# Performance work log

Measured on AMD Instinct MI355X. Metric: run time of the kernel, lower is better.

Reference implementation:

```python
import jax, jax.numpy as jnp
import numpy as np

B, H, L, PRED_LEN = 512, 512, 2, 256


def setup_inputs() -> dict:
    key = jax.random.key(0)
    ks = jax.random.split(key, 12)
    s = 1.0 / np.sqrt(H)  # PyTorch LSTM init scale
    f32 = jnp.float32
    return {
        "h": jax.random.normal(ks[0], (L, B, H), f32),
        "c": jax.random.normal(ks[1], (L, B, H), f32),
        "W_ih0": jax.random.normal(ks[2], (4 * H, 1), f32) * s,
        "W_hh0": jax.random.normal(ks[3], (4 * H, H), f32) * s,
        "b_ih0": jax.random.normal(ks[4], (4 * H,), f32) * s,
        "b_hh0": jax.random.normal(ks[5], (4 * H,), f32) * s,
        "W_ih1": jax.random.normal(ks[6], (4 * H, H), f32) * s,
        "W_hh1": jax.random.normal(ks[7], (4 * H, H), f32) * s,
        "b_ih1": jax.random.normal(ks[8], (4 * H,), f32) * s,
        "b_hh1": jax.random.normal(ks[9], (4 * H,), f32) * s,
        "fc_w": jax.random.normal(ks[10], (1, H), f32) * s,
        "fc_b": jax.random.normal(ks[11], (1,), f32) * s,
        "pred_len": PRED_LEN,
    }


def _lstm_cell(x, h, c, W_ih, W_hh, b_ih, b_hh):
    # PyTorch gate order: i, f, g, o
    gates = x @ W_ih.T + h @ W_hh.T + (b_ih + b_hh)
    i, f, g, o = jnp.split(gates, 4, axis=-1)
    c_new = jax.nn.sigmoid(f) * c + jax.nn.sigmoid(i) * jnp.tanh(g)
    h_new = jax.nn.sigmoid(o) * jnp.tanh(c_new)
    return h_new, c_new


def reference(h, c, W_ih0, W_hh0, b_ih0, b_hh0, W_ih1, W_hh1, b_ih1, b_hh1,
              fc_w, fc_b, pred_len):
    params = ((W_ih0, W_hh0, b_ih0, b_hh0), (W_ih1, W_hh1, b_ih1, b_hh1))
    Bsz = h.shape[1]

    def step(carry, _):
        x, hs, cs = carry  # x: (B,1); hs, cs: (L,B,H)
        inp = x
        new_h, new_c = [], []
        for l in range(len(params)):
            hn, cn = _lstm_cell(inp, hs[l], cs[l], *params[l])
            new_h.append(hn)
            new_c.append(cn)
            inp = hn
        pred = inp @ fc_w.T + fc_b  # (B,1)
        return (pred, jnp.stack(new_h), jnp.stack(new_c)), pred[:, 0]

    x0 = jnp.zeros((Bsz, 1), h.dtype)  # torch.zeros(B,1,1) start token
    _, preds = jax.lax.scan(step, (x0, h, c), None, length=pred_len)
    return preds.T  # (B, pred_len)
```

## Files before the change

kernel.cpp:

```cpp
#include <hip/hip_runtime.h>
#include <hip/hip_bf16.h>


#define B_ 512
#define H_ 512
#define T_ 256
#define NWG 256
#define NTHR 512

typedef _Float16 half8_t __attribute__((ext_vector_type(8)));
typedef _Float16 half4_t __attribute__((ext_vector_type(4)));
typedef _Float16 half2_t __attribute__((ext_vector_type(2)));
typedef float floatx4 __attribute__((ext_vector_type(4)));

#define W16_BYTES  (3u * 4u * H_ * H_ * 2u)
#define HBUF_ELEMS (B_ * H_)
#define HBUF_BYTES (HBUF_ELEMS * 2u)
#define H0_OFF   ((size_t)W16_BYTES)
#define H1_OFF   (H0_OFF + 2 * HBUF_BYTES)
#define BAR_OFF  (H1_OFF + 2 * HBUF_BYTES)
#define PART_OFF (BAR_OFF + 2048)

__device__ __forceinline__ float sigm_(float x) { return 1.0f / (1.0f + __expf(-x)); }
__device__ __forceinline__ float tanh_(float x) { return 1.0f - 2.0f / (1.0f + __expf(2.0f * x)); }

__global__ void prep_weights(const float* __restrict__ whh0,
                             const float* __restrict__ wih1,
                             const float* __restrict__ whh1,
                             _Float16* __restrict__ w16) {
    const int QM = (4 * H_ * H_) / 4;
    int i = blockIdx.x * blockDim.x + threadIdx.x;
    if (i >= 3 * QM) return;
    const float* src; int base;
    if (i < QM)          { src = whh0; base = 0; }
    else if (i < 2 * QM) { src = wih1; base = QM; }
    else                 { src = whh1; base = 2 * QM; }
    float4 v = ((const float4*)src)[i - base];
    half4_t h;
    h[0] = (_Float16)v.x; h[1] = (_Float16)v.y; h[2] = (_Float16)v.z; h[3] = (_Float16)v.w;
    ((half4_t*)w16)[i] = h;
}

__global__ void prep_state(const float* __restrict__ h_in,
                           _Float16* __restrict__ H0, _Float16* __restrict__ H1) {
    int i = blockIdx.x * blockDim.x + threadIdx.x;
    float4 a = ((const float4*)h_in)[i];
    float4 b = ((const float4*)h_in)[(B_ * H_) / 4 + i];
    half4_t ha, hb;
    ha[0] = (_Float16)a.x; ha[1] = (_Float16)a.y; ha[2] = (_Float16)a.z; ha[3] = (_Float16)a.w;
    hb[0] = (_Float16)b.x; hb[1] = (_Float16)b.y; hb[2] = (_Float16)b.z; hb[3] = (_Float16)b.w;
    ((half4_t*)H0)[i] = ha;
    ((half4_t*)H1)[i] = hb;
}

#define GLL16(gptr, lptr) __builtin_amdgcn_global_load_lds( \
    (const __attribute__((address_space(1))) unsigned int*)(gptr), \
    (__attribute__((address_space(3))) unsigned int*)(lptr), 16, 0, 0x01)

__device__ __forceinline__ void stage_rows(const char* gsrc, char* lbuf, int wv, int lane) {
#pragma unroll
    for (int i = 0; i < 8; ++i) {
        int row = wv * 8 + i;
        const char* g_ = gsrc + row * 1024 + (((lane ^ (row & 7)) & 63) << 4);
        GLL16(g_, lbuf + row * 1024);
    }
}

__device__ __forceinline__ floatx4 load16_sc0(const float* p) {
    floatx4 v;
    asm volatile("global_load_dwordx4 %0, %1, off sc0" : "=v"(v) : "v"(p) : "memory");
    return v;
}

#define LBAR() asm volatile("s_waitcnt lgkmcnt(0)\n\ts_barrier" ::: "memory")
#define FBAR() asm volatile("s_waitcnt vmcnt(0) lgkmcnt(0)\n\ts_barrier" ::: "memory")

__launch_bounds__(NTHR)
__global__ void lstm_decode(
    const float* __restrict__ c_in,
    const float* __restrict__ wih0, const float* __restrict__ bih0,
    const float* __restrict__ bhh0,
    const float* __restrict__ bih1, const float* __restrict__ bhh1,
    const float* __restrict__ fcw, const float* __restrict__ fcb,
    const _Float16* __restrict__ w16,
    _Float16* __restrict__ Hs0, _Float16* __restrict__ Hs1,
    int* __restrict__ bar, float* __restrict__ part,
    float* __restrict__ outp)
{
    __shared__ __align__(16) char bufA[65536];
    __shared__ __align__(16) char bufB[65536];
    __shared__ float gbuf[4][64][20];
    __shared__ float xrow[64];
    __shared__ int sh_bt, sh_ct;

    const int tid  = (int)threadIdx.x;
    const int lane = tid & 63;
    const int wv   = tid >> 6;
    const int g    = wv & 3;
    const int kh   = wv >> 2;
    const int cl   = lane & 15;
    const int kg   = lane >> 4;

    if (tid == 0) {
        unsigned int xcc;
        asm volatile("s_getreg_b32 %0, hwreg(HW_REG_XCC_ID)" : "=s"(xcc));
        int mybt = (int)(xcc & 7u);
        int rank = atomicAdd(&bar[256 + mybt], 1);
        sh_bt = mybt;
        sh_ct = rank & 31;
    }
    __syncthreads();
    const int bt = sh_bt;
    const int ct = sh_ct;

    const int n = g * H_ + ct * 16 + cl;
    half8_t wf0[8], wf1[8], wf2[8];
    {
        const _Float16* r0 = w16 + (size_t)n * H_ + kh * 256 + kg * 8;
        const _Float16* r1 = r0 + 4 * H_ * H_;
        const _Float16* r2 = r0 + 8 * H_ * H_;
#pragma unroll
        for (int ksg = 0; ksg < 8; ++ksg) {
            wf0[ksg] = *(const half8_t*)(r0 + ksg * 32);
            wf1[ksg] = *(const half8_t*)(r1 + ksg * 32);
            wf2[ksg] = *(const half8_t*)(r2 + ksg * 32);
        }
    }
    const float b0   = bih0[n] + bhh0[n];
    const float b1   = bih1[n] + bhh1[n];
    const float wx   = wih0[n];
    const float fcb0 = fcb[0];

    const int erow = tid >> 3;
    const int ecol = (tid & 7) * 2;
    float c0a, c0b, c1a, c1b;
    {
        size_t base0 = (size_t)(bt * 64 + erow) * H_ + ct * 16 + ecol;
        c0a = c_in[base0];                     c0b = c_in[base0 + 1];
        c1a = c_in[(size_t)B_ * H_ + base0];   c1b = c_in[(size_t)B_ * H_ + base0 + 1];
    }
    const float2 fcv = *(const float2*)(fcw + ct * 16 + ecol);

    const int abase = cl * 1024 + kh * 512 + kg * 16;
    const int axor  = (cl & 7) << 4;

    int* flagg   = bar + bt * 32;
    float* partg = part + bt * 2048;
    int ep = 0;

#define PASSH(bufc, wf, acc, M0, M1) do {                                     \
    _Pragma("unroll")                                                         \
    for (int ksg = 0; ksg < 8; ++ksg) {                                       \
        _Pragma("unroll")                                                     \
        for (int mt = (M0); mt <= (M1); ++mt) {                               \
            int a_ = (abase + mt * 16384 + ksg * 64) ^ axor;                  \
            half8_t av_ = *(const half8_t*)((bufc) + a_);                     \
            acc[mt] = __builtin_amdgcn_mfma_f32_16x16x32_f16(av_, (wf)[ksg],  \
                                                             acc[mt], 0, 0, 0); \
        }                                                                     \
    }                                                                         \
} while (0)

    floatx4 accG0[4], accG1[4];
    floatx4 pv;

    if (tid < 64) xrow[tid] = 0.f;
    stage_rows((const char*)Hs0 + (size_t)bt * 64 * 1024, bufB, wv, lane);
    stage_rows((const char*)Hs1 + (size_t)bt * 64 * 1024, bufA, wv, lane);
    FBAR();
#pragma unroll
    for (int mt = 0; mt < 4; ++mt) accG0[mt] = (floatx4)0.f;
    PASSH(bufB, wf0, accG0, 0, 3);

    for (int t = 0; t < T_; ++t) {
        const size_t pnxt = (size_t)((t + 1) & 1);
        _Float16* h0w = Hs0 + pnxt * HBUF_ELEMS;
        _Float16* h1w = Hs1 + pnxt * HBUF_ELEMS;

        if (t > 0) {
            asm volatile("s_waitcnt vmcnt(8)" : "+v"(pv) :: "memory");
            float xs = (pv[0] + pv[1]) + (pv[2] + pv[3]);
            xs += __shfl_xor(xs, 1);
            xs += __shfl_xor(xs, 2);
            xs += __shfl_xor(xs, 4);
            xs += fcb0;
            if ((tid & 7) == 0) {
                xrow[tid >> 3] = xs;
                if (ct == 0) outp[(size_t)(bt * 64 + (tid >> 3)) * T_ + (t - 1)] = xs;
            }
        }
        LBAR();

        if (kh == 0) {
#pragma unroll
            for (int mt = 0; mt < 4; ++mt)
#pragma unroll
                for (int r = 0; r < 4; ++r)
                    gbuf[g][mt * 16 + kg * 4 + r][cl] =
                        accG0[mt][r] + __builtin_fmaf(xrow[mt * 16 + kg * 4 + r], wx, b0);
        }
        LBAR();
        if (kh == 1) {
#pragma unroll
            for (int mt = 0; mt < 4; ++mt)
#pragma unroll
                for (int r = 0; r < 4; ++r)
                    gbuf[g][mt * 16 + kg * 4 + r][cl] += accG0[mt][r];
        }
        LBAR();

        {
            float2 iv = *(const float2*)&gbuf[0][erow][ecol];
            float2 fv = *(const float2*)&gbuf[1][erow][ecol];
            float2 gv = *(const float2*)&gbuf[2][erow][ecol];
            float2 ov = *(const float2*)&gbuf[3][erow][ecol];
            float ca = sigm_(fv.x) * c0a + sigm_(iv.x) * tanh_(gv.x);
            float cb = sigm_(fv.y) * c0b + sigm_(iv.y) * tanh_(gv.y);
            c0a = ca; c0b = cb;
            half2_t hh;
            hh[0] = (_Float16)(sigm_(ov.x) * tanh_(ca));
            hh[1] = (_Float16)(sigm_(ov.y) * tanh_(cb));
            *(half2_t*)(h0w + (size_t)(bt * 64 + erow) * H_ + ct * 16 + ecol) = hh;
        }

        ++ep;
        FBAR();
        if (tid == 0)
            __hip_atomic_store(&flagg[ct], ep, __ATOMIC_RELAXED, __HIP_MEMORY_SCOPE_AGENT);

#pragma unroll
        for (int mt = 0; mt < 4; ++mt) {
            if (kh == 0) {
#pragma unroll
                for (int r = 0; r < 4; ++r) accG1[mt][r] = b1;
            } else {
                accG1[mt] = (floatx4)0.f;
            }
        }
        PASSH(bufA, wf2, accG1, 0, 1);

        if (wv == 0) {
            for (;;) {
                int v_ = __hip_atomic_load(&flagg[lane & 31], __ATOMIC_RELAXED,
                                           __HIP_MEMORY_SCOPE_AGENT);
                if (__all(v_ >= ep)) break;
            }
        }
        __syncthreads();

        stage_rows((const char*)h0w + (size_t)bt * 64 * 1024, bufB, wv, lane);

        PASSH(bufA, wf2, accG1, 2, 3);

        FBAR();

        PASSH(bufB, wf1, accG1, 0, 3);

        if (kh == 0) {
#pragma unroll
            for (int mt = 0; mt < 4; ++mt)
#pragma unroll
                for (int r = 0; r < 4; ++r)
                    gbuf[g][mt * 16 + kg * 4 + r][cl] = accG1[mt][r];
        }
        LBAR();
        if (kh == 1) {
#pragma unroll
            for (int mt = 0; mt < 4; ++mt)
#pragma unroll
                for (int r = 0; r < 4; ++r)
                    gbuf[g][mt * 16 + kg * 4 + r][cl] += accG1[mt][r];
        }
        LBAR();

        {
            float2 iv = *(const float2*)&gbuf[0][erow][ecol];
            float2 fv = *(const float2*)&gbuf[1][erow][ecol];
            float2 gv = *(const float2*)&gbuf[2][erow][ecol];
            float2 ov = *(const float2*)&gbuf[3][erow][ecol];
            float ca = sigm_(fv.x) * c1a + sigm_(iv.x) * tanh_(gv.x);
            float cb = sigm_(fv.y) * c1b + sigm_(iv.y) * tanh_(gv.y);
            c1a = ca; c1b = cb;
            float ha = sigm_(ov.x) * tanh_(ca);
            float hb = sigm_(ov.y) * tanh_(cb);
            half2_t hh; hh[0] = (_Float16)ha; hh[1] = (_Float16)hb;
            *(half2_t*)(h1w + (size_t)(bt * 64 + erow) * H_ + ct * 16 + ecol) = hh;
            float ps = __builtin_fmaf(ha, fcv.x, hb * fcv.y);
            ps += __shfl_xor(ps, 1);
            ps += __shfl_xor(ps, 2);
            ps += __shfl_xor(ps, 4);
            if ((tid & 7) == 0)
                partg[(tid >> 3) * 32 + ct] = ps;
        }

        ++ep;
        FBAR();
        if (tid == 0)
            __hip_atomic_store(&flagg[ct], ep, __ATOMIC_RELAXED, __HIP_MEMORY_SCOPE_AGENT);

#pragma unroll
        for (int mt = 0; mt < 4; ++mt) accG0[mt] = (floatx4)0.f;
        PASSH(bufB, wf0, accG0, 0, 1);

        if (wv == 0) {
            for (;;) {
                int v_ = __hip_atomic_load(&flagg[lane & 31], __ATOMIC_RELAXED,
                                           __HIP_MEMORY_SCOPE_AGENT);
                if (__all(v_ >= ep)) break;
            }
        }
        __syncthreads();

        pv = load16_sc0(partg + (tid >> 3) * 32 + (tid & 7) * 4);
        stage_rows((const char*)Hs1 + pnxt * HBUF_BYTES + (size_t)bt * 64 * 1024,
                   bufA, wv, lane);

        PASSH(bufB, wf0, accG0, 2, 3);
    }

    {
        asm volatile("s_waitcnt vmcnt(8)" : "+v"(pv) :: "memory");
        float xs = (pv[0] + pv[1]) + (pv[2] + pv[3]);
        xs += __shfl_xor(xs, 1);
        xs += __shfl_xor(xs, 2);
        xs += __shfl_xor(xs, 4);
        xs += fcb0;
        if ((tid & 7) == 0 && ct == 0)
            outp[(size_t)(bt * 64 + (tid >> 3)) * T_ + (T_ - 1)] = xs;
    }
#undef PASSH
#undef LBAR
#undef FBAR
}

extern "C" void kernel_launch(void* const* d_in, const int* in_sizes, int n_in,
                              void* d_out, int out_size, void* d_ws, size_t ws_size,
                              hipStream_t stream) {
    const float* h_in = (const float*)d_in[0];
    const float* c_in = (const float*)d_in[1];
    const float* wih0 = (const float*)d_in[2];
    const float* whh0 = (const float*)d_in[3];
    const float* bih0 = (const float*)d_in[4];
    const float* bhh0 = (const float*)d_in[5];
    const float* wih1 = (const float*)d_in[6];
    const float* whh1 = (const float*)d_in[7];
    const float* bih1 = (const float*)d_in[8];
    const float* bhh1 = (const float*)d_in[9];
    const float* fcw  = (const float*)d_in[10];
    const float* fcb  = (const float*)d_in[11];
    float* out = (float*)d_out;

    char* ws = (char*)d_ws;
    _Float16* w16 = (_Float16*)ws;
    _Float16* Hs0 = (_Float16*)(ws + H0_OFF);
    _Float16* Hs1 = (_Float16*)(ws + H1_OFF);
    int* bar      = (int*)(ws + BAR_OFF);
    float* part   = (float*)(ws + PART_OFF);

    (void)hipMemsetAsync(bar, 0, 2048, stream);

    {
        const int n4 = 3 * (4 * H_ * H_) / 4;
        prep_weights<<<(n4 + 255) / 256, 256, 0, stream>>>(whh0, wih1, whh1, w16);
    }
    prep_state<<<(B_ * H_ / 4) / 256, 256, 0, stream>>>(h_in, Hs0, Hs1);

    lstm_decode<<<NWG, NTHR, 0, stream>>>(c_in, wih0, bih0, bhh0, bih1, bhh1,
                                          fcw, fcb, w16, Hs0, Hs1, bar, part, out);
}
```

Baseline: 1.809 ms.

## Remap waves to two gates per quarter-K so each LDS A-fragment feeds two MFMAs

```diff
diff --git a/kernel.cpp b/kernel.cpp
--- a/kernel.cpp
+++ b/kernel.cpp
@@ -89,17 +89,19 @@
 {
     __shared__ __align__(16) char bufA[65536];
     __shared__ __align__(16) char bufB[65536];
-    __shared__ float gbuf[4][64][20];
     __shared__ float xrow[64];
     __shared__ int sh_bt, sh_ct;
 
     const int tid  = (int)threadIdx.x;
     const int lane = tid & 63;
     const int wv   = tid >> 6;
-    const int g    = wv & 3;
-    const int kh   = wv >> 2;
+    const int gp_  = wv & 1;
+    const int kq   = wv >> 1;
     const int cl   = lane & 15;
     const int kg   = lane >> 4;
+
+    float (*gbB)[2][64][20] = (float (*)[2][64][20])bufB;
+    float (*gbA)[2][64][20] = (float (*)[2][64][20])bufA;
 
     if (tid == 0) {
         unsigned int xcc;
@@ -113,22 +115,24 @@
     const int bt = sh_bt;
     const int ct = sh_ct;
 
-    const int n = g * H_ + ct * 16 + cl;
-    half8_t wf0[8], wf1[8], wf2[8];
-    {
-        const _Float16* r0 = w16 + (size_t)n * H_ + kh * 256 + kg * 8;
+    half8_t wf0[2][4], wf1[2][4], wf2[2][4];
+    float b0v[2], b1v[2], wxv[2];
+#pragma unroll
+    for (int g = 0; g < 2; ++g) {
+        const int n = (gp_ + 2 * g) * H_ + ct * 16 + cl;
+        const _Float16* r0 = w16 + (size_t)n * H_ + kq * 128 + kg * 8;
         const _Float16* r1 = r0 + 4 * H_ * H_;
         const _Float16* r2 = r0 + 8 * H_ * H_;
 #pragma unroll
-        for (int ksg = 0; ksg < 8; ++ksg) {
-            wf0[ksg] = *(const half8_t*)(r0 + ksg * 32);
-            wf1[ksg] = *(const half8_t*)(r1 + ksg * 32);
-            wf2[ksg] = *(const half8_t*)(r2 + ksg * 32);
-        }
-    }
-    const float b0   = bih0[n] + bhh0[n];
-    const float b1   = bih1[n] + bhh1[n];
-    const float wx   = wih0[n];
+        for (int ksg = 0; ksg < 4; ++ksg) {
+            wf0[g][ksg] = *(const half8_t*)(r0 + ksg * 32);
+            wf1[g][ksg] = *(const half8_t*)(r1 + ksg * 32);
+            wf2[g][ksg] = *(const half8_t*)(r2 + ksg * 32);
+        }
+        b0v[g] = bih0[n] + bhh0[n];
+        b1v[g] = bih1[n] + bhh1[n];
+        wxv[g] = wih0[n];
+    }
     const float fcb0 = fcb[0];
 
     const int erow = tid >> 3;
@@ -141,27 +145,29 @@
     }
     const float2 fcv = *(const float2*)(fcw + ct * 16 + ecol);
 
-    const int abase = cl * 1024 + kh * 512 + kg * 16;
+    const int abase = cl * 1024 + kq * 256 + kg * 16;
     const int axor  = (cl & 7) << 4;
 
     int* flagg   = bar + bt * 32;
     float* partg = part + bt * 2048;
     int ep = 0;
 
-#define PASSH(bufc, wf, acc, M0, M1) do {                                     \
+#define PASSH(bufc, wfm, acc, M0, M1) do {                                    \
     _Pragma("unroll")                                                         \
-    for (int ksg = 0; ksg < 8; ++ksg) {                                       \
+    for (int ksg = 0; ksg < 4; ++ksg) {                                       \
         _Pragma("unroll")                                                     \
         for (int mt = (M0); mt <= (M1); ++mt) {                               \
             int a_ = (abase + mt * 16384 + ksg * 64) ^ axor;                  \
             half8_t av_ = *(const half8_t*)((bufc) + a_);                     \
-            acc[mt] = __builtin_amdgcn_mfma_f32_16x16x32_f16(av_, (wf)[ksg],  \
-                                                             acc[mt], 0, 0, 0); \
+            _Pragma("unroll")                                                 \
+            for (int g = 0; g < 2; ++g)                                       \
+                acc[g][mt] = __builtin_amdgcn_mfma_f32_16x16x32_f16(          \
+                    av_, (wfm)[g][ksg], acc[g][mt], 0, 0, 0);                 \
         }                                                                     \
     }                                                                         \
 } while (0)
 
-    floatx4 accG0[4], accG1[4];
+    floatx4 accG0[2][4], accG1[2][4];
     floatx4 pv;
 
     if (tid < 64) xrow[tid] = 0.f;
@@ -169,7 +175,9 @@
     stage_rows((const char*)Hs1 + (size_t)bt * 64 * 1024, bufA, wv, lane);
     FBAR();
 #pragma unroll
-    for (int mt = 0; mt < 4; ++mt) accG0[mt] = (floatx4)0.f;
+    for (int g = 0; g < 2; ++g)
+#pragma unroll
+        for (int mt = 0; mt < 4; ++mt) accG0[g][mt] = (floatx4)0.f;
     PASSH(bufB, wf0, accG0, 0, 3);
 
     for (int t = 0; t < T_; ++t) {
@@ -191,35 +199,50 @@
         }
         LBAR();
 
-        if (kh == 0) {
-#pragma unroll
-            for (int mt = 0; mt < 4; ++mt)
-#pragma unroll
-                for (int r = 0; r < 4; ++r)
-                    gbuf[g][mt * 16 + kg * 4 + r][cl] =
-                        accG0[mt][r] + __builtin_fmaf(xrow[mt * 16 + kg * 4 + r], wx, b0);
+        if (kq & 1) {
+#pragma unroll
+            for (int g = 0; g < 2; ++g)
+#pragma unroll
+                for (int mt = 0; mt < 4; ++mt)
+#pragma unroll
+                    for (int r = 0; r < 4; ++r)
+                        gbB[gp_ + 2 * g][kq >> 1][mt * 16 + kg * 4 + r][cl] = accG0[g][mt][r];
         }
         LBAR();
-        if (kh == 1) {
-#pragma unroll
-            for (int mt = 0; mt < 4; ++mt)
-#pragma unroll
-                for (int r = 0; r < 4; ++r)
-                    gbuf[g][mt * 16 + kg * 4 + r][cl] += accG0[mt][r];
+        if (!(kq & 1)) {
+#pragma unroll
+            for (int g = 0; g < 2; ++g)
+#pragma unroll
+                for (int mt = 0; mt < 4; ++mt)
+#pragma unroll
+                    for (int r = 0; r < 4; ++r) {
+                        float v_ = accG0[g][mt][r];
+                        if (kq == 0)
+                            v_ += __builtin_fmaf(xrow[mt * 16 + kg * 4 + r], wxv[g], b0v[g]);
+                        gbB[gp_ + 2 * g][kq >> 1][mt * 16 + kg * 4 + r][cl] += v_;
+                    }
         }
         LBAR();
 
         {
-            float2 iv = *(const float2*)&gbuf[0][erow][ecol];
-            float2 fv = *(const float2*)&gbuf[1][erow][ecol];
-            float2 gv = *(const float2*)&gbuf[2][erow][ecol];
-            float2 ov = *(const float2*)&gbuf[3][erow][ecol];
-            float ca = sigm_(fv.x) * c0a + sigm_(iv.x) * tanh_(gv.x);
-            float cb = sigm_(fv.y) * c0b + sigm_(iv.y) * tanh_(gv.y);
+            float2 iv0 = *(const float2*)&gbB[0][0][erow][ecol];
+            float2 iv1 = *(const float2*)&gbB[0][1][erow][ecol];
+            float2 fv0 = *(const float2*)&gbB[1][0][erow][ecol];
+            float2 fv1 = *(const float2*)&gbB[1][1][erow][ecol];
+            float2 gv0 = *(const float2*)&gbB[2][0][erow][ecol];
+            float2 gv1 = *(const float2*)&gbB[2][1][erow][ecol];
+            float2 ov0 = *(const float2*)&gbB[3][0][erow][ecol];
+            float2 ov1 = *(const float2*)&gbB[3][1][erow][ecol];
+            float ix = iv0.x + iv1.x, iy = iv0.y + iv1.y;
+            float fx = fv0.x + fv1.x, fy = fv0.y + fv1.y;
+            float qx = gv0.x + gv1.x, qy = gv0.y + gv1.y;
+            float ox = ov0.x + ov1.x, oy = ov0.y + ov1.y;
+            float ca = sigm_(fx) * c0a + sigm_(ix) * tanh_(qx);
+            float cb = sigm_(fy) * c0b + sigm_(iy) * tanh_(qy);
             c0a = ca; c0b = cb;
             half2_t hh;
-            hh[0] = (_Float16)(sigm_(ov.x) * tanh_(ca));
-            hh[1] = (_Float16)(sigm_(ov.y) * tanh_(cb));
+            hh[0] = (_Float16)(sigm_(ox) * tanh_(ca));
+            hh[1] = (_Float16)(sigm_(oy) * tanh_(cb));
             *(half2_t*)(h0w + (size_t)(bt * 64 + erow) * H_ + ct * 16 + ecol) = hh;
         }
 
@@ -229,14 +252,9 @@
             __hip_atomic_store(&flagg[ct], ep, __ATOMIC_RELAXED, __HIP_MEMORY_SCOPE_AGENT);
 
 #pragma unroll
-        for (int mt = 0; mt < 4; ++mt) {
-            if (kh == 0) {
-#pragma unroll
-                for (int r = 0; r < 4; ++r) accG1[mt][r] = b1;
-            } else {
-                accG1[mt] = (floatx4)0.f;
-            }
-        }
+        for (int g = 0; g < 2; ++g)
+#pragma unroll
+            for (int mt = 0; mt < 4; ++mt) accG1[g][mt] = (floatx4)0.f;
         PASSH(bufA, wf2, accG1, 0, 1);
 
         if (wv == 0) {
@@ -256,33 +274,48 @@
 
         PASSH(bufB, wf1, accG1, 0, 3);
 
-        if (kh == 0) {
-#pragma unroll
-            for (int mt = 0; mt < 4; ++mt)
-#pragma unroll
-                for (int r = 0; r < 4; ++r)
-                    gbuf[g][mt * 16 + kg * 4 + r][cl] = accG1[mt][r];
+        if (kq & 1) {
+#pragma unroll
+            for (int g = 0; g < 2; ++g)
+#pragma unroll
+                for (int mt = 0; mt < 4; ++mt)
+#pragma unroll
+                    for (int r = 0; r < 4; ++r)
+                        gbA[gp_ + 2 * g][kq >> 1][mt * 16 + kg * 4 + r][cl] = accG1[g][mt][r];
         }
         LBAR();
-        if (kh == 1) {
-#pragma unroll
-            for (int mt = 0; mt < 4; ++mt)
-#pragma unroll
-                for (int r = 0; r < 4; ++r)
-                    gbuf[g][mt * 16 + kg * 4 + r][cl] += accG1[mt][r];
+        if (!(kq & 1)) {
+#pragma unroll
+            for (int g = 0; g < 2; ++g)
+#pragma unroll
+                for (int mt = 0; mt < 4; ++mt)
+#pragma unroll
+                    for (int r = 0; r < 4; ++r) {
+                        float v_ = accG1[g][mt][r];
+                        if (kq == 0) v_ += b1v[g];
+                        gbA[gp_ + 2 * g][kq >> 1][mt * 16 + kg * 4 + r][cl] += v_;
+                    }
         }
         LBAR();
 
         {
-            float2 iv = *(const float2*)&gbuf[0][erow][ecol];
-            float2 fv = *(const float2*)&gbuf[1][erow][ecol];
-            float2 gv = *(const float2*)&gbuf[2][erow][ecol];
-            float2 ov = *(const float2*)&gbuf[3][erow][ecol];
-            float ca = sigm_(fv.x) * c1a + sigm_(iv.x) * tanh_(gv.x);
-            float cb = sigm_(fv.y) * c1b + sigm_(iv.y) * tanh_(gv.y);
+            float2 iv0 = *(const float2*)&gbA[0][0][erow][ecol];
+            float2 iv1 = *(const float2*)&gbA[0][1][erow][ecol];
+            float2 fv0 = *(const float2*)&gbA[1][0][erow][ecol];
+            float2 fv1 = *(const float2*)&gbA[1][1][erow][ecol];
+            float2 gv0 = *(const float2*)&gbA[2][0][erow][ecol];
+            float2 gv1 = *(const float2*)&gbA[2][1][erow][ecol];
+            float2 ov0 = *(const float2*)&gbA[3][0][erow][ecol];
+            float2 ov1 = *(const float2*)&gbA[3][1][erow][ecol];
+            float ix = iv0.x + iv1.x, iy = iv0.y + iv1.y;
+            float fx = fv0.x + fv1.x, fy = fv0.y + fv1.y;
+            float qx = gv0.x + gv1.x, qy = gv0.y + gv1.y;
+            float ox = ov0.x + ov1.x, oy = ov0.y + ov1.y;
+            float ca = sigm_(fx) * c1a + sigm_(ix) * tanh_(qx);
+            float cb = sigm_(fy) * c1b + sigm_(iy) * tanh_(qy);
             c1a = ca; c1b = cb;
-            float ha = sigm_(ov.x) * tanh_(ca);
-            float hb = sigm_(ov.y) * tanh_(cb);
+            float ha = sigm_(ox) * tanh_(ca);
+            float hb = sigm_(oy) * tanh_(cb);
             half2_t hh; hh[0] = (_Float16)ha; hh[1] = (_Float16)hb;
             *(half2_t*)(h1w + (size_t)(bt * 64 + erow) * H_ + ct * 16 + ecol) = hh;
             float ps = __builtin_fmaf(ha, fcv.x, hb * fcv.y);
@@ -299,7 +332,9 @@
             __hip_atomic_store(&flagg[ct], ep, __ATOMIC_RELAXED, __HIP_MEMORY_SCOPE_AGENT);
 
 #pragma unroll
-        for (int mt = 0; mt < 4; ++mt) accG0[mt] = (floatx4)0.f;
+        for (int g = 0; g < 2; ++g)
+#pragma unroll
+            for (int mt = 0; mt < 4; ++mt) accG0[g][mt] = (floatx4)0.f;
         PASSH(bufB, wf0, accG0, 0, 1);
 
         if (wv == 0) {
```

Measured after the change: 2.370 ms. +31.0%, slower.
